# Performance work log

Measured on AMD Instinct MI355X. Metric: run time of the kernel, lower is better.

## Reference

```python
import jax, jax.numpy as jnp
import numpy as np

HEADS = 8
B, N, DIM = 8, 1024, 128  # n must be a perfect square (H=W=32)
LN_EPS = 1e-5


def _region_means(xg):
    """Four-quadrant region means per position via integral image.
    xg: [b,H,W,d] -> [b,H,W,4,d]. For position (h,w) the torch code pools:
      r1 = x[:, :h+1, :w+1], r2 = x[:, :h+1, w:], r3 = x[:, h:, :w+1], r4 = x[:, h:, w:]
    """
    b, H, W, d = xg.shape
    # padded 2D prefix sum: P[:, i, j] = sum over rows<i, cols<j
    P = jnp.pad(jnp.cumsum(jnp.cumsum(xg, axis=1), axis=2),
                ((0, 0), (1, 0), (1, 0), (0, 0)))
    r1 = P[:, 1:, 1:]                                              # sum x[:h+1,:w+1]
    r2 = P[:, 1:, -1:] - P[:, 1:, :-1]                             # sum x[:h+1, w:]
    r3 = P[:, -1:, 1:] - P[:, :-1, 1:]                             # sum x[h:, :w+1]
    r4 = P[:, -1:, -1:] - P[:, :-1, -1:] - P[:, -1:, :-1] + P[:, :-1, :-1]
    ah = jnp.arange(H, dtype=xg.dtype)
    aw = jnp.arange(W, dtype=xg.dtype)
    hp1 = (ah + 1.0)[:, None]   # h+1
    wp1 = (aw + 1.0)[None, :]   # w+1
    hr = (H - ah)[:, None]      # H-h
    wr = (W - aw)[None, :]      # W-w
    c1 = (hp1 * wp1)[None, :, :, None]
    c2 = (hp1 * wr)[None, :, :, None]
    c3 = (hr * wp1)[None, :, :, None]
    c4 = (hr * wr)[None, :, :, None]
    return jnp.stack([r1 / c1, r2 / c2, r3 / c3, r4 / c4], axis=3)


def setup_inputs() -> dict:
    key = jax.random.key(0)
    ks = jax.random.split(key, 10)
    s = 0.02
    return {
        "x": jax.random.normal(ks[0], (B, N, DIM), jnp.float32),
        "ln_g": jnp.ones((DIM,), jnp.float32),
        "ln_b": jnp.zeros((DIM,), jnp.float32),
        "Wqkv": jax.random.normal(ks[1], (DIM, 3 * HEADS * DIM), jnp.float32) * s,
        "bqkv": jax.random.normal(ks[2], (3 * HEADS * DIM,), jnp.float32) * s,
        "Wq": jax.random.normal(ks[3], (DIM, DIM), jnp.float32) * s,
        "Wk": jax.random.normal(ks[4], (DIM, DIM), jnp.float32) * s,
        "Wv": jax.random.normal(ks[5], (DIM, DIM), jnp.float32) * s,
        "Wo": jax.random.normal(ks[6], (DIM, DIM), jnp.float32) * s,
        "bo": jax.random.normal(ks[7], (DIM,), jnp.float32) * s,
        "Wout": jax.random.normal(ks[8], (HEADS * DIM, DIM), jnp.float32) * s,
        "bout": jax.random.normal(ks[9], (DIM,), jnp.float32) * s,
    }


def reference(x, ln_g, ln_b, Wqkv, bqkv, Wq, Wk, Wv, Wo, bo, Wout, bout):
    b, n, dim = x.shape
    H = W = int(n ** 0.5)
    # LayerNorm
    mu = jnp.mean(x, axis=-1, keepdims=True)
    var = jnp.mean(jnp.square(x - mu), axis=-1, keepdims=True)
    xn = (x - mu) * jax.lax.rsqrt(var + LN_EPS) * ln_g + ln_b
    # qkv projection; only q is actually used downstream (k,v chunks are dead)
    qkv = xn @ Wqkv + bqkv
    q = qkv[..., : HEADS * dim].reshape(b, n, HEADS, dim).transpose(0, 2, 1, 3)  # [b,h,n,d]
    # region features, identical across heads -> keep unbroadcast [b,n,4,d]
    regions = _region_means(xn.reshape(b, H, W, dim)).reshape(b, n, 4, dim)
    # RegionAggregator
    qh = q @ Wq                                   # [b,h,n,d]
    k = jnp.einsum('bnrd,de->bnre', regions, Wk)  # [b,n,4,d]
    v = jnp.einsum('bnrd,de->bnre', regions, Wv)
    scale = (dim // HEADS) ** -0.5
    attn = jax.nn.softmax(jnp.einsum('bhnd,bnrd->bhnr', qh, k) * scale, axis=-1)
    agg = jnp.einsum('bhnr,bnrd->bhnd', attn, v)
    out = agg @ Wo + bo                           # [b,h,n,d]
    out = out.transpose(0, 2, 1, 3).reshape(b, n, HEADS * dim)
    return out @ Wout + bout
```

## Files before the change

kernel.cpp:

```cpp
#include <hip/hip_runtime.h>
#include <hip/hip_bf16.h>
#include <stdint.h>

#define HEADS 8
#define NN 1024
#define DIM 128
#define HW 32
#define LN_EPS 1e-5f

typedef __hip_bfloat16 bf16;
typedef __bf16 bf16x8 __attribute__((ext_vector_type(8)));
typedef float floatx4 __attribute__((ext_vector_type(4)));

__device__ __forceinline__ float b2f(bf16 v){ return __bfloat162float(v); }
__device__ __forceinline__ bf16 f2b(float v){ return __float2bfloat16(v); }

__device__ __forceinline__ float ldin(const void* p, size_t i, int f){
    return f ? ((const float*)p)[i] : b2f(((const bf16*)p)[i]);
}
__device__ __forceinline__ float4 ldin4(const void* p, size_t i, int f){
    if (f) return *reinterpret_cast<const float4*>((const float*)p + i);
    ushort4 u = *reinterpret_cast<const ushort4*>((const bf16*)p + i);
    float4 r;
    r.x = b2f(*(bf16*)&u.x); r.y = b2f(*(bf16*)&u.y);
    r.z = b2f(*(bf16*)&u.z); r.w = b2f(*(bf16*)&u.w);
    return r;
}
__device__ __forceinline__ int dtf(const void* g){
    return (((const uint32_t*)g)[0] == 0x3F800000u) ? 1 : 0;
}

__global__ __launch_bounds__(256) void lnscan_kernel(const void* __restrict__ x,
                                                     const void* __restrict__ g,
                                                     const void* __restrict__ bta,
                                                     bf16* __restrict__ xn,
                                                     float* __restrict__ P){
    __shared__ float lnv[32][128];
    int f = dtf(g);
    int b = blockIdx.x >> 5, hh = blockIdx.x & 31;
    int wv = threadIdx.x >> 6, lane = threadIdx.x & 63;
    float gl0 = ldin(g, lane, f),    gl1 = ldin(g, lane+64, f);
    float bl0 = ldin(bta, lane, f),  bl1 = ldin(bta, lane+64, f);
    size_t rowbase = (size_t)b*NN + (size_t)hh*HW;
#pragma unroll
    for (int rnd=0; rnd<8; rnd++){
        int w = rnd*4 + wv;
        size_t base = (rowbase + w)*DIM;
        float v0 = ldin(x, base+lane,    f);
        float v1 = ldin(x, base+lane+64, f);
        float s = v0+v1, ss = v0*v0+v1*v1;
        for (int o=32;o;o>>=1){ s += __shfl_xor(s,o,64); ss += __shfl_xor(ss,o,64); }
        float mu = s * (1.0f/DIM);
        float var = ss * (1.0f/DIM) - mu*mu;
        float rs = rsqrtf(var + LN_EPS);
        float y0 = (v0-mu)*rs*gl0 + bl0;
        float y1 = (v1-mu)*rs*gl1 + bl1;
        xn[base+lane]    = f2b(y0);
        xn[base+lane+64] = f2b(y1);
        lnv[w][lane]    = y0;
        lnv[w][lane+64] = y1;
    }
    __syncthreads();
    if (threadIdx.x < 128){
        int c = threadIdx.x;
        float run = 0.f;
        float* Pr = P + rowbase*DIM + c;
#pragma unroll
        for (int w=0; w<HW; w++){
            run += lnv[w][c];
            Pr[(size_t)w*DIM] = run;
        }
    }
}

__global__ __launch_bounds__(128) void colscan_kernel(float* __restrict__ P){
    int b = blockIdx.x >> 5, w = blockIdx.x & 31, c = threadIdx.x;
    float* Pc = P + ((size_t)(b*NN + w))*DIM + c;
    float run = 0.f;
    for (int h=0; h<HW; h++){
        size_t o = (size_t)h*HW*DIM;
        run += Pc[o]; Pc[o] = run;
    }
}

__global__ __launch_bounds__(256) void prep_kernel(const void* __restrict__ Wqkv,
                                                   const void* __restrict__ bqkv,
                                                   const void* __restrict__ Wq,
                                                   const void* __restrict__ Wk,
                                                   const void* __restrict__ Wv,
                                                   const void* __restrict__ Wo,
                                                   const void* __restrict__ bo,
                                                   const void* __restrict__ Wout,
                                                   const void* __restrict__ ln_g,
                                                   bf16* __restrict__ WhT,
                                                   bf16* __restrict__ WhoT,
                                                   bf16* __restrict__ WkvT,
                                                   float* __restrict__ bq,
                                                   float* __restrict__ bfin_part){
    __shared__ float S1[128][132];
    __shared__ float S2[8][132];
    int f = dtf(ln_g);
    int t = threadIdx.x;
    int blk = blockIdx.x;
    if (blk < 128){
        int h = blk >> 4, dc = blk & 15;
#pragma unroll
        for (int i=0;i<16;i++){
            int idx4 = (t + i*256)*4;
            int k = idx4 >> 7, e = idx4 & 127;
            *reinterpret_cast<float4*>(&S1[k][e]) = ldin4(Wq, idx4, f);
        }
        {
            int idx4 = t*4;
            int dl = idx4 >> 7, k = idx4 & 127;
            *reinterpret_cast<float4*>(&S2[dl][k]) =
                ldin4(Wqkv, (size_t)(dc*8+dl)*3072 + h*128 + k, f);
        }
        __syncthreads();
        int d = t & 7;
        int e0 = (t >> 3) * 4;
        float acc[4] = {0.f,0.f,0.f,0.f};
        for (int k=0;k<128;k++){
            float a = S2[d][k];
            float4 wv = *reinterpret_cast<const float4*>(&S1[k][e0]);
            acc[0] += a*wv.x; acc[1] += a*wv.y; acc[2] += a*wv.z; acc[3] += a*wv.w;
        }
#pragma unroll
        for (int i=0;i<4;i++)
            WhT[(size_t)(h*128 + e0 + i)*128 + dc*8 + d] = f2b(acc[i]);
    } else if (blk < 256){
        int h = (blk-128) >> 4, dc = (blk-128) & 15;
#pragma unroll
        for (int i=0;i<16;i++){
            int idx4 = (t + i*256)*4;
            int k = idx4 >> 7, e = idx4 & 127;
            *reinterpret_cast<float4*>(&S1[k][e]) =
                ldin4(Wout, (size_t)(h*128 + k)*128 + e, f);
        }
        {
            int idx4 = t*4;
            int dl = idx4 >> 7, k = idx4 & 127;
            *reinterpret_cast<float4*>(&S2[dl][k]) =
                ldin4(Wo, (size_t)(dc*8+dl)*128 + k, f);
        }
        __syncthreads();
        int d = t & 7;
        int e0 = (t >> 3) * 4;
        float acc[4] = {0.f,0.f,0.f,0.f};
        for (int k=0;k<128;k++){
            float a = S2[d][k];
            float4 wv = *reinterpret_cast<const float4*>(&S1[k][e0]);
            acc[0] += a*wv.x; acc[1] += a*wv.y; acc[2] += a*wv.z; acc[3] += a*wv.w;
        }
#pragma unroll
        for (int i=0;i<4;i++)
            WhoT[(size_t)(e0 + i)*1024 + h*128 + dc*8 + d] = f2b(acc[i]);
    } else {
        int sub = blk - 256;
        if (sub < 8){
            int h = sub;
            int e = t & 127, kh = t >> 7;
            float s = 0.f;
            for (int k=kh*64; k<kh*64+64; k++)
                s += ldin(bqkv, h*128 + k, f) * ldin(Wq, (size_t)k*128 + e, f);
            S1[kh][e] = s;
            __syncthreads();
            if (t < 128) bq[h*128 + t] = S1[0][t] + S1[1][t];
        } else if (sub < 16){
            int h = sub - 8;
            if (t < 128) S2[0][t] = ldin(bo, t, f);
            __syncthreads();
            int e = t & 127, half = t >> 7;
            float s = 0.f;
            for (int k = half*64; k < half*64 + 64; k++)
                s += S2[0][k] * ldin(Wout, (size_t)(h*128 + k)*128 + e, f);
            S1[half][e] = s;
            __syncthreads();
            if (t < 128) bfin_part[h*128 + t] = S1[0][t] + S1[1][t];
        } else {
            const void* W = (sub == 16) ? Wk : Wv;
            int base = (sub == 16) ? 0 : 128;
#pragma unroll
            for (int i=0;i<16;i++){
                int idx4 = (t + i*256)*4;
                int d = idx4 >> 7, e = idx4 & 127;
                *reinterpret_cast<float4*>(&S1[d][e]) = ldin4(W, idx4, f);
            }
            __syncthreads();
            for (int i=0;i<64;i++){
                int idx = t + i*256; int e = idx >> 7, d = idx & 127;
                WkvT[(size_t)(base + e)*128 + d] = f2b(S1[d][e]);
            }
        }
    }
}

__global__ __launch_bounds__(256) void attn_fused_kernel(const float* __restrict__ P,
                                                         const bf16* __restrict__ WkvT,
                                                         const bf16* __restrict__ WhT,
                                                         const bf16* __restrict__ WhoT,
                                                         const float* __restrict__ bq,
                                                         const float* __restrict__ bfin_part,
                                                         const void* __restrict__ bout,
                                                         const bf16* __restrict__ xn,
                                                         const void* __restrict__ ln_g,
                                                         void* __restrict__ out){
    __shared__ __align__(16) char pool[56576];
    bf16 (*As)[136]     = reinterpret_cast<bf16(*)[136]>(pool);
    bf16 (*kS)[16][136] = reinterpret_cast<bf16(*)[16][136]>(pool);
    bf16 (*vS)[16][136] = reinterpret_cast<bf16(*)[16][136]>(pool);
    bf16 (*Bs)[136]     = reinterpret_cast<bf16(*)[136]>(pool + 17408);
    bf16 (*qL)[136]     = reinterpret_cast<bf16(*)[136]>(pool + 17408);
    float* logits       = reinterpret_cast<float*>(pool + 21760);
    float4* probsS      = reinterpret_cast<float4*>(pool + 23808);
    bf16 (*xnS)[136]    = reinterpret_cast<bf16(*)[136]>(pool + 52224);

    int f = dtf(ln_g);
    int t = threadIdx.x;
    int bn0 = blockIdx.x * 16;
    {
        int bn_local = t >> 4;
        int c0 = (t & 15) * 8;
        int bn = bn0 + bn_local;
        int b = bn >> 10, n = bn & 1023;
        int hh = n >> 5, ww = n & 31;
        const float* Pb = P + (size_t)b*NN*DIM;
        auto ld8 = [&](int h, int w, float* o){
            if (h==0 || w==0){
#pragma unroll
                for (int j=0;j<8;j++) o[j] = 0.f;
                return;
            }
            const float* p = Pb + ((size_t)((h-1)*HW + (w-1)))*DIM + c0;
            float4 u = *reinterpret_cast<const float4*>(p);
            float4 v = *reinterpret_cast<const float4*>(p+4);
            o[0]=u.x;o[1]=u.y;o[2]=u.z;o[3]=u.w;o[4]=v.x;o[5]=v.y;o[6]=v.z;o[7]=v.w;
        };
        float f_h1 = (float)(hh+1), f_w1 = (float)(ww+1);
        float f_hr = (float)(HW-hh), f_wr = (float)(HW-ww);
        float a0[8], a1[8];
        ld8(hh+1, ww+1, a0);
#pragma unroll
        for (int j=0;j<8;j++) As[bn_local*4 + 0][c0+j] = f2b(a0[j] / (f_h1*f_w1));
        ld8(hh+1, HW, a0); ld8(hh+1, ww, a1);
#pragma unroll
        for (int j=0;j<8;j++) As[bn_local*4 + 1][c0+j] = f2b((a0[j]-a1[j]) / (f_h1*f_wr));
        ld8(HW, ww+1, a0); ld8(hh, ww+1, a1);
#pragma unroll
        for (int j=0;j<8;j++) As[bn_local*4 + 2][c0+j] = f2b((a0[j]-a1[j]) / (f_hr*f_w1));
        float a2[8], a3[8];
        ld8(HW, HW, a0); ld8(hh, HW, a1); ld8(HW, ww, a2); ld8(hh, ww, a3);
#pragma unroll
        for (int j=0;j<8;j++)
            As[bn_local*4 + 3][c0+j] = f2b((a0[j]-a1[j]-a2[j]+a3[j]) / (f_hr*f_wr));
        *reinterpret_cast<uint4*>(&xnS[t >> 4][(t & 15)*8]) =
            *reinterpret_cast<const uint4*>(&xn[(size_t)(bn0 + (t >> 4))*DIM + (t & 15)*8]);
    }
    int w = t >> 6, lane = t & 63;
    int r = lane & 15, q = lane >> 4;
    floatx4 acc[16];
#pragma unroll
    for (int i=0;i<16;i++) acc[i] = (floatx4){0.f,0.f,0.f,0.f};
    for (int half=0; half<2; half++){
        __syncthreads();
#pragma unroll
        for (int i=0;i<8;i++){
            int id = t + i*256;
            int row = id >> 4, c8 = id & 15;
            *reinterpret_cast<uint4*>(&Bs[row][c8*8]) =
                *reinterpret_cast<const uint4*>(&WkvT[(size_t)(half*128 + row)*128 + c8*8]);
        }
        __syncthreads();
#pragma unroll
        for (int kc=0;kc<4;kc++){
            bf16x8 a = *reinterpret_cast<const bf16x8*>(&As[w*16 + r][kc*32 + q*8]);
#pragma unroll
            for (int nt=0;nt<8;nt++){
                bf16x8 b = *reinterpret_cast<const bf16x8*>(&Bs[nt*16 + r][kc*32 + q*8]);
                acc[half*8+nt] = __builtin_amdgcn_mfma_f32_16x16x32_bf16(a, b, acc[half*8+nt], 0, 0, 0);
            }
        }
    }
    __syncthreads();
#pragma unroll
    for (int nt=0;nt<8;nt++){
#pragma unroll
        for (int i=0;i<4;i++){
            int rowg = w*16 + q*4 + i;
            kS[rowg & 3][rowg >> 2][nt*16 + r] = f2b(acc[nt][i]);
        }
    }
    for (int h=0; h<8; h++){
        floatx4 qa[2];
        qa[0] = (floatx4){0.f,0.f,0.f,0.f};
        qa[1] = (floatx4){0.f,0.f,0.f,0.f};
#pragma unroll
        for (int kc=0;kc<4;kc++){
            bf16x8 a = *reinterpret_cast<const bf16x8*>(&xnS[r][kc*32 + q*8]);
#pragma unroll
            for (int nl=0;nl<2;nl++){
                int e = (w*2 + nl)*16 + r;
                bf16x8 b = *reinterpret_cast<const bf16x8*>(
                    &WhT[((size_t)(h*128 + e))*128 + kc*32 + q*8]);
                qa[nl] = __builtin_amdgcn_mfma_f32_16x16x32_bf16(a, b, qa[nl], 0, 0, 0);
            }
        }
        __syncthreads();
#pragma unroll
        for (int nl=0;nl<2;nl++){
            int col = (w*2 + nl)*16 + r;
            float bb = bq[h*128 + col];
#pragma unroll
            for (int i=0;i<4;i++)
                qL[q*4 + i][col] = f2b(qa[nl][i] + bb);
        }
        __syncthreads();
        {
            floatx4 s = (floatx4){0.f,0.f,0.f,0.f};
#pragma unroll
            for (int kc=0;kc<4;kc++){
                bf16x8 a = *reinterpret_cast<const bf16x8*>(&qL[r][kc*32 + q*8]);
                bf16x8 b = *reinterpret_cast<const bf16x8*>(&kS[w][r][kc*32 + q*8]);
                s = __builtin_amdgcn_mfma_f32_16x16x32_bf16(a, b, s, 0, 0, 0);
            }
            if ((r >> 2) == q){
                int i = r & 3;
                float d = (i==0)?s[0]:(i==1)?s[1]:(i==2)?s[2]:s[3];
                logits[(r*8 + h)*4 + w] = d;
            }
        }
    }
    __syncthreads();
    if (t < 128){
        int bn = t >> 3, h = t & 7;
        const float* L = &logits[(bn*8 + h)*4];
        float l0 = L[0]*0.25f, l1 = L[1]*0.25f, l2 = L[2]*0.25f, l3 = L[3]*0.25f;
        float m = fmaxf(fmaxf(l0,l1),fmaxf(l2,l3));
        float e0 = __expf(l0-m), e1=__expf(l1-m), e2=__expf(l2-m), e3=__expf(l3-m);
        float inv = 1.0f/(e0+e1+e2+e3);
        probsS[bn*8 + h] = (float4){e0*inv, e1*inv, e2*inv, e3*inv};
    }
#pragma unroll
    for (int nt=0;nt<8;nt++){
#pragma unroll
        for (int i=0;i<4;i++){
            int rowg = w*16 + q*4 + i;
            vS[rowg & 3][rowg >> 2][nt*16 + r] = f2b(acc[8+nt][i]);
        }
    }
    __syncthreads();
    floatx4 oacc[2];
    oacc[0] = (floatx4){0.f,0.f,0.f,0.f};
    oacc[1] = (floatx4){0.f,0.f,0.f,0.f};
    for (int h=0; h<8; h++){
        float4 pv = *reinterpret_cast<const float4*>(&probsS[r*8 + h]);
#pragma unroll
        for (int kc=0;kc<4;kc++){
            int c = kc*32 + q*8;
            bf16x8 v0 = *reinterpret_cast<const bf16x8*>(&vS[0][r][c]);
            bf16x8 v1 = *reinterpret_cast<const bf16x8*>(&vS[1][r][c]);
            bf16x8 v2 = *reinterpret_cast<const bf16x8*>(&vS[2][r][c]);
            bf16x8 v3 = *reinterpret_cast<const bf16x8*>(&vS[3][r][c]);
            bf16x8 a;
#pragma unroll
            for (int j=0;j<8;j++){
                float s = pv.x*(float)v0[j] + pv.y*(float)v1[j]
                        + pv.z*(float)v2[j] + pv.w*(float)v3[j];
                a[j] = (__bf16)s;
            }
#pragma unroll
            for (int nl=0;nl<2;nl++){
                int e = (w*2 + nl)*16 + r;
                bf16x8 b = *reinterpret_cast<const bf16x8*>(
                    &WhoT[(size_t)e*1024 + h*128 + kc*32 + q*8]);
                oacc[nl] = __builtin_amdgcn_mfma_f32_16x16x32_bf16(a, b, oacc[nl], 0, 0, 0);
            }
        }
    }
#pragma unroll
    for (int nl=0;nl<2;nl++){
        int col = (w*2 + nl)*16 + r;
        float bias = ldin(bout, col, f);
#pragma unroll
        for (int h=0;h<8;h++) bias += bfin_part[h*128 + col];
#pragma unroll
        for (int i=0;i<4;i++){
            int row = bn0 + q*4 + i;
            float v = oacc[nl][i] + bias;
            if (f) ((float*)out)[(size_t)row*DIM + col] = v;
            else   ((bf16*)out)[(size_t)row*DIM + col] = f2b(v);
        }
    }
}

extern "C" void kernel_launch(void* const* d_in, const int* in_sizes, int n_in,
                              void* d_out, int out_size, void* d_ws, size_t ws_size,
                              hipStream_t stream){
    const void* x    = d_in[0];
    const void* ln_g = d_in[1];
    const void* ln_b = d_in[2];
    const void* Wqkv = d_in[3];
    const void* bqkv = d_in[4];
    const void* Wq   = d_in[5];
    const void* Wk   = d_in[6];
    const void* Wv   = d_in[7];
    const void* Wo   = d_in[8];
    const void* bo   = d_in[9];
    const void* Wout = d_in[10];
    const void* bout = d_in[11];

    char* ws = (char*)d_ws;
    size_t off = 0;
    auto alloc = [&](size_t bytes)->char*{
        char* p = ws + off; off += (bytes + 255) & ~size_t(255); return p;
    };
    bf16*  WhT   = (bf16*)alloc((size_t)1024*128*2);
    bf16*  WkvT  = (bf16*)alloc((size_t)256*128*2);
    bf16*  WhoT  = (bf16*)alloc((size_t)128*1024*2);
    float* bq    = (float*)alloc(1024*4);
    float* bfin_part = (float*)alloc(8*128*4);
    float* P     = (float*)alloc((size_t)8*NN*DIM*4);
    bf16*  xn    = (bf16*)alloc((size_t)8192*128*2);

    prep_kernel<<<274, 256, 0, stream>>>(Wqkv, bqkv, Wq, Wk, Wv, Wo, bo, Wout,
                                         ln_g, WhT, WhoT, WkvT, bq, bfin_part);
    lnscan_kernel<<<256, 256, 0, stream>>>(x, ln_g, ln_b, xn, P);
    colscan_kernel<<<256, 128, 0, stream>>>(P);
    attn_fused_kernel<<<512, 256, 0, stream>>>(P, WkvT, WhT, WhoT, bq, bfin_part,
                                               bout, xn, ln_g, d_out);
}
```

Baseline: 147.0 us.

## Batch four heads per q-projection pass and give k, v and q separate LDS regions

The per-head loop in the fused attention kernel now handles four heads per group, so the q-projection MFMAs for four heads issue together and only two barrier pairs are needed instead of eight. k fragments are held in registers, and v is stored to its own LDS region early instead of overwriting k later. The PV loop is reordered to load each v tile once and reuse it across all eight heads, with the probabilities kept in registers. This raises LDS use and register pressure, which may lower occupancy.

Result: no change. 147.3 us (+0.2%).

```diff
diff --git a/kernel.cpp b/kernel.cpp
--- a/kernel.cpp
+++ b/kernel.cpp
@@ -205,15 +205,15 @@
                                                          const bf16* __restrict__ xn,
                                                          const void* __restrict__ ln_g,
                                                          void* __restrict__ out){
-    __shared__ __align__(16) char pool[56576];
+    __shared__ __align__(16) char pool[59136];
     bf16 (*As)[136]     = reinterpret_cast<bf16(*)[136]>(pool);
     bf16 (*kS)[16][136] = reinterpret_cast<bf16(*)[16][136]>(pool);
-    bf16 (*vS)[16][136] = reinterpret_cast<bf16(*)[16][136]>(pool);
     bf16 (*Bs)[136]     = reinterpret_cast<bf16(*)[136]>(pool + 17408);
-    bf16 (*qL)[136]     = reinterpret_cast<bf16(*)[136]>(pool + 17408);
-    float* logits       = reinterpret_cast<float*>(pool + 21760);
-    float4* probsS      = reinterpret_cast<float4*>(pool + 23808);
+    bf16 (*qL)[16][136] = reinterpret_cast<bf16(*)[16][136]>(pool + 17408);
+    bf16 (*vS)[16][136] = reinterpret_cast<bf16(*)[16][136]>(pool + 34816);
     bf16 (*xnS)[136]    = reinterpret_cast<bf16(*)[136]>(pool + 52224);
+    float* logits       = reinterpret_cast<float*>(pool + 56576);
+    float4* probsS      = reinterpret_cast<float4*>(pool + 57088);
 
     int f = dtf(ln_g);
     int t = threadIdx.x;
@@ -288,45 +288,59 @@
         for (int i=0;i<4;i++){
             int rowg = w*16 + q*4 + i;
             kS[rowg & 3][rowg >> 2][nt*16 + r] = f2b(acc[nt][i]);
-        }
-    }
-    for (int h=0; h<8; h++){
-        floatx4 qa[2];
-        qa[0] = (floatx4){0.f,0.f,0.f,0.f};
-        qa[1] = (floatx4){0.f,0.f,0.f,0.f};
+            vS[rowg & 3][rowg >> 2][nt*16 + r] = f2b(acc[8+nt][i]);
+        }
+    }
+    __syncthreads();
+    bf16x8 kf[4];
+#pragma unroll
+    for (int kc=0;kc<4;kc++)
+        kf[kc] = *reinterpret_cast<const bf16x8*>(&kS[w][r][kc*32 + q*8]);
+    for (int g=0; g<2; g++){
+        floatx4 qa[4][2];
+#pragma unroll
+        for (int hh=0;hh<4;hh++){ qa[hh][0]=(floatx4){0,0,0,0}; qa[hh][1]=(floatx4){0,0,0,0}; }
 #pragma unroll
         for (int kc=0;kc<4;kc++){
             bf16x8 a = *reinterpret_cast<const bf16x8*>(&xnS[r][kc*32 + q*8]);
 #pragma unroll
+            for (int hh=0;hh<4;hh++){
+                int h = g*4 + hh;
+#pragma unroll
+                for (int nl=0;nl<2;nl++){
+                    int e = (w*2 + nl)*16 + r;
+                    bf16x8 b = *reinterpret_cast<const bf16x8*>(
+                        &WhT[((size_t)(h*128 + e))*128 + kc*32 + q*8]);
+                    qa[hh][nl] = __builtin_amdgcn_mfma_f32_16x16x32_bf16(a, b, qa[hh][nl], 0, 0, 0);
+                }
+            }
+        }
+        __syncthreads();
+#pragma unroll
+        for (int hh=0;hh<4;hh++){
+            int h = g*4 + hh;
+#pragma unroll
             for (int nl=0;nl<2;nl++){
-                int e = (w*2 + nl)*16 + r;
-                bf16x8 b = *reinterpret_cast<const bf16x8*>(
-                    &WhT[((size_t)(h*128 + e))*128 + kc*32 + q*8]);
-                qa[nl] = __builtin_amdgcn_mfma_f32_16x16x32_bf16(a, b, qa[nl], 0, 0, 0);
-            }
-        }
-        __syncthreads();
-#pragma unroll
-        for (int nl=0;nl<2;nl++){
-            int col = (w*2 + nl)*16 + r;
-            float bb = bq[h*128 + col];
-#pragma unroll
-            for (int i=0;i<4;i++)
-                qL[q*4 + i][col] = f2b(qa[nl][i] + bb);
-        }
-        __syncthreads();
-        {
+                int col = (w*2 + nl)*16 + r;
+                float bb = bq[h*128 + col];
+#pragma unroll
+                for (int i=0;i<4;i++)
+                    qL[hh][q*4 + i][col] = f2b(qa[hh][nl][i] + bb);
+            }
+        }
+        __syncthreads();
+#pragma unroll
+        for (int hh=0;hh<4;hh++){
             floatx4 s = (floatx4){0.f,0.f,0.f,0.f};
 #pragma unroll
             for (int kc=0;kc<4;kc++){
-                bf16x8 a = *reinterpret_cast<const bf16x8*>(&qL[r][kc*32 + q*8]);
-                bf16x8 b = *reinterpret_cast<const bf16x8*>(&kS[w][r][kc*32 + q*8]);
-                s = __builtin_amdgcn_mfma_f32_16x16x32_bf16(a, b, s, 0, 0, 0);
+                bf16x8 a = *reinterpret_cast<const bf16x8*>(&qL[hh][r][kc*32 + q*8]);
+                s = __builtin_amdgcn_mfma_f32_16x16x32_bf16(a, kf[kc], s, 0, 0, 0);
             }
             if ((r >> 2) == q){
                 int i = r & 3;
                 float d = (i==0)?s[0]:(i==1)?s[1]:(i==2)?s[2]:s[3];
-                logits[(r*8 + h)*4 + w] = d;
+                logits[(r*8 + g*4 + hh)*4 + w] = d;
             }
         }
     }
@@ -340,32 +354,27 @@
         float inv = 1.0f/(e0+e1+e2+e3);
         probsS[bn*8 + h] = (float4){e0*inv, e1*inv, e2*inv, e3*inv};
     }
-#pragma unroll
-    for (int nt=0;nt<8;nt++){
-#pragma unroll
-        for (int i=0;i<4;i++){
-            int rowg = w*16 + q*4 + i;
-            vS[rowg & 3][rowg >> 2][nt*16 + r] = f2b(acc[8+nt][i]);
-        }
-    }
     __syncthreads();
+    float4 pv[8];
+#pragma unroll
+    for (int h=0;h<8;h++) pv[h] = probsS[r*8 + h];
     floatx4 oacc[2];
     oacc[0] = (floatx4){0.f,0.f,0.f,0.f};
     oacc[1] = (floatx4){0.f,0.f,0.f,0.f};
-    for (int h=0; h<8; h++){
-        float4 pv = *reinterpret_cast<const float4*>(&probsS[r*8 + h]);
-#pragma unroll
-        for (int kc=0;kc<4;kc++){
-            int c = kc*32 + q*8;
-            bf16x8 v0 = *reinterpret_cast<const bf16x8*>(&vS[0][r][c]);
-            bf16x8 v1 = *reinterpret_cast<const bf16x8*>(&vS[1][r][c]);
-            bf16x8 v2 = *reinterpret_cast<const bf16x8*>(&vS[2][r][c]);
-            bf16x8 v3 = *reinterpret_cast<const bf16x8*>(&vS[3][r][c]);
+#pragma unroll
+    for (int kc=0;kc<4;kc++){
+        int c = kc*32 + q*8;
+        bf16x8 v0 = *reinterpret_cast<const bf16x8*>(&vS[0][r][c]);
+        bf16x8 v1 = *reinterpret_cast<const bf16x8*>(&vS[1][r][c]);
+        bf16x8 v2 = *reinterpret_cast<const bf16x8*>(&vS[2][r][c]);
+        bf16x8 v3 = *reinterpret_cast<const bf16x8*>(&vS[3][r][c]);
+#pragma unroll
+        for (int h=0; h<8; h++){
             bf16x8 a;
 #pragma unroll
             for (int j=0;j<8;j++){
-                float s = pv.x*(float)v0[j] + pv.y*(float)v1[j]
-                        + pv.z*(float)v2[j] + pv.w*(float)v3[j];
+                float s = pv[h].x*(float)v0[j] + pv[h].y*(float)v1[j]
+                        + pv[h].z*(float)v2[j] + pv[h].w*(float)v3[j];
                 a[j] = (__bf16)s;
             }
 #pragma unroll
```
